# Kernel optimization log

Measured on AMD Instinct MI355X. Metric: run time of the kernel, lower is better.

## Reference

```python
import jax, jax.numpy as jnp
import numpy as np

B, T, H, V, L = 128, 64, 256, 128, 2


def _gru_layer(x_seq, w_ih, w_hh, b_ih, b_hh):
    """PyTorch-convention GRU layer. x_seq: (B,T,Hin) -> (B,T,H), h_last (B,H)."""
    # Precompute input projections once for all timesteps: (B,T,3H)
    xp = jnp.einsum('bti,gi->btg', x_seq, w_ih) + b_ih

    def step(h, xp_t):
        hp = h @ w_hh.T + b_hh                      # (B,3H)
        xr, xz, xn = jnp.split(xp_t, 3, axis=-1)
        hr, hz, hn = jnp.split(hp, 3, axis=-1)
        r = jax.nn.sigmoid(xr + hr)
        z = jax.nn.sigmoid(xz + hz)
        n = jnp.tanh(xn + r * hn)
        h_new = (1.0 - z) * n + z * h
        return h_new, h_new

    h0 = jnp.zeros((x_seq.shape[0], w_hh.shape[1]), x_seq.dtype)
    h_last, ys = jax.lax.scan(step, h0, jnp.swapaxes(xp, 0, 1))  # scan over T
    return jnp.swapaxes(ys, 0, 1), h_last


def setup_inputs() -> dict:
    key = jax.random.key(0)
    ks = jax.random.split(key, 16)
    s = 1.0 / np.sqrt(H)

    def u(k, shape):
        return jax.random.uniform(k, shape, jnp.float32, -s, s)

    x = jax.random.randint(ks[0], (B, T), 0, V)
    embed = jax.random.normal(ks[1], (V, H), jnp.float32) * 0.02
    embed = embed.at[0].set(0.0)  # padding_idx=0
    return {
        'x': x,
        'embed': embed,
        'w_ih0': u(ks[2], (3 * H, H)), 'w_hh0': u(ks[3], (3 * H, H)),
        'b_ih0': u(ks[4], (3 * H,)),   'b_hh0': u(ks[5], (3 * H,)),
        'w_ih1': u(ks[6], (3 * H, H)), 'w_hh1': u(ks[7], (3 * H, H)),
        'b_ih1': u(ks[8], (3 * H,)),   'b_hh1': u(ks[9], (3 * H,)),
        'W_a': u(ks[10], (H, H)),
        'U_a': u(ks[11], (H, H)),
        'v_a': u(ks[12], (H,)),
        'fc_W': u(ks[13], (V, 2 * H)),
        'fc_b': u(ks[14], (V,)),
    }


def reference(x, embed, w_ih0, w_hh0, b_ih0, b_hh0,
              w_ih1, w_hh1, b_ih1, b_hh1,
              W_a, U_a, v_a, fc_W, fc_b):
    # Embedding (dropout is identity in eval-mode reference)
    emb = embed[x]                                   # (B,T,H)
    h1_seq, _ = _gru_layer(emb, w_ih0, w_hh0, b_ih0, b_hh0)
    enc, h_last = _gru_layer(h1_seq, w_ih1, w_hh1, b_ih1, b_hh1)  # (B,T,H)

    # Vectorized per-step Bahdanau attention: queries are enc itself (h_t = enc[:,t])
    Wa_e = enc @ W_a.T                               # (B,T,H) keys, computed once
    Ua_h = enc @ U_a.T                               # (B,T,H) queries
    energy = jnp.einsum('btkh,h->btk',
                        jnp.tanh(Wa_e[:, None, :, :] + Ua_h[:, :, None, :]), v_a)
    alpha = jax.nn.softmax(energy, axis=-1)          # (B,T,T)
    ctx = jnp.einsum('btk,bkh->bth', alpha, enc)     # (B,T,H)

    combined = jnp.concatenate([enc, ctx], axis=-1)  # (B,T,2H)
    logits = combined @ fc_W.T + fc_b                # (B,T,V)
    return logits, h_last
```

## Files before the change

### kernel.cpp

```cpp
#include <hip/hip_runtime.h>
#include <math.h>

#define BB 128
#define TT 64
#define HH 256
#define G3 768
#define VV 128

typedef _Float16 half8 __attribute__((ext_vector_type(8)));
typedef float f32x4 __attribute__((ext_vector_type(4)));

__global__ __launch_bounds__(256) void pack_whh_f16(const float* __restrict__ w,
                                                    _Float16* __restrict__ out) {
    int d = blockIdx.x * 256 + threadIdx.x;
    int e   = d & 7;
    int l   = (d >> 3) & 63;
    int kap = (d >> 9) & 7;
    int wt  = d >> 12;
    int wv  = wt / 6, tau = wt % 6;
    int ncol = (tau >> 1) * 256 + wv * 32 + (tau & 1) * 16 + (l & 15);
    int k    = kap * 32 + (l >> 4) * 8 + e;
    out[d] = (_Float16)w[ncol * HH + k];
}

__global__ __launch_bounds__(256) void prep_bias(const float* __restrict__ b_ih,
                                                 const float* __restrict__ b_hh,
                                                 float* __restrict__ outb) {
    int j = blockIdx.x * 256 + threadIdx.x;
    outb[j] = b_ih[j] + (j < 2 * HH ? b_hh[j] : 0.f);
}

__global__ __launch_bounds__(256) void gemm_bt(
    const float* __restrict__ A1, int lda1, int K1,
    const float* __restrict__ A2, int lda2, int K2,
    const float* __restrict__ Bw, int ldb,
    const float* __restrict__ bias,
    float* __restrict__ C, int ldc, int M, int N)
{
    __shared__ alignas(16) float As[16][68];
    __shared__ alignas(16) float Bs[16][68];
    const int tid = threadIdx.x;
    const int lc = tid & 15, lr = tid >> 4;
    const int ty = tid >> 4, tx = tid & 15;
    const int row0 = blockIdx.y * 64, col0 = blockIdx.x * 64;
    float acc[4][4] = {};
    const int KT = K1 + K2;

    for (int k0 = 0; k0 < KT; k0 += 16) {
        const float* Ap; int lda, kk0;
        if (k0 < K1) { Ap = A1; lda = lda1; kk0 = k0; }
        else         { Ap = A2; lda = lda2; kk0 = k0 - K1; }
#pragma unroll
        for (int r = 0; r < 4; ++r) {
            As[lc][lr + 16 * r] = Ap[(row0 + lr + 16 * r) * lda + kk0 + lc];
            Bs[lc][lr + 16 * r] = Bw[(col0 + lr + 16 * r) * ldb + k0 + lc];
        }
        __syncthreads();
#pragma unroll
        for (int kk = 0; kk < 16; ++kk) {
            const float4 a4 = *(const float4*)&As[kk][ty * 4];
            const float4 b4 = *(const float4*)&Bs[kk][tx * 4];
            const float av[4] = {a4.x, a4.y, a4.z, a4.w};
            const float bv[4] = {b4.x, b4.y, b4.z, b4.w};
#pragma unroll
            for (int i = 0; i < 4; ++i)
#pragma unroll
                for (int j = 0; j < 4; ++j)
                    acc[i][j] += av[i] * bv[j];
        }
        __syncthreads();
    }

    float bv[4];
#pragma unroll
    for (int j = 0; j < 4; ++j)
        bv[j] = bias ? bias[col0 + tx * 4 + j] : 0.f;
#pragma unroll
    for (int i = 0; i < 4; ++i) {
        const int r = row0 + ty * 4 + i;
        float4 o;
        o.x = acc[i][0] + bv[0];
        o.y = acc[i][1] + bv[1];
        o.z = acc[i][2] + bv[2];
        o.w = acc[i][3] + bv[3];
        *(float4*)&C[r * ldc + col0 + tx * 4] = o;
    }
}

__global__ __launch_bounds__(512, 2) void gru_mfma(
    const _Float16* __restrict__ wp,
    const float* __restrict__ b_hh,
    const float* __restrict__ xsrc,
    const int*   __restrict__ xidx,
    float* __restrict__ out_seq,
    float* __restrict__ hlast,
    int mode)
{
    __shared__ alignas(16) _Float16 hbuf[16][264];
    __shared__ int tok[16][TT];
    const int tid = threadIdx.x;
    const int wv = tid >> 6, l = tid & 63;
    const int l15 = l & 15, lhi = l >> 4;
    const int r0 = blockIdx.x * 16;

    for (int i = tid; i < 16 * 264; i += 512) ((_Float16*)hbuf)[i] = (_Float16)0.f;
    if (mode == 0) {
        ((int*)tok)[tid]       = xidx[r0 * TT + tid];
        ((int*)tok)[tid + 512] = xidx[r0 * TT + tid + 512];
    }

    half8 W[48];
    const half8* wp8 = (const half8*)wp;
    const int fb = wv * 48 * 64;
#pragma unroll
    for (int f = 0; f < 48; ++f) W[f] = wp8[fb + f * 64 + l];

    const int colbase = wv * 32 + l15;
    const float bhn0 = b_hh[2 * HH + colbase];
    const float bhn1 = b_hh[2 * HH + colbase + 16];
    float hold[2][4] = {};
    __syncthreads();

    for (int t = 0; t < TT; ++t) {
        f32x4 acc[6];
#pragma unroll
        for (int tau = 0; tau < 6; ++tau) acc[tau] = (f32x4)0.f;

#pragma unroll
        for (int kap = 0; kap < 8; ++kap) {
            const half8 a = *(const half8*)&hbuf[l15][kap * 32 + lhi * 8];
#pragma unroll
            for (int tau = 0; tau < 6; ++tau)
                acc[tau] = __builtin_amdgcn_mfma_f32_16x16x32_f16(
                    a, W[tau * 8 + kap], acc[tau], 0, 0, 0);
        }
        __syncthreads();

#pragma unroll
        for (int s = 0; s < 2; ++s) {
            const int col = colbase + s * 16;
            const float bhn = s ? bhn1 : bhn0;
            float xr[4], xz[4], xn[4];
#pragma unroll
            for (int reg = 0; reg < 4; ++reg) {
                const int rr = lhi * 4 + reg;
                const long base = (mode == 0)
                    ? (long)tok[rr][t] * G3
                    : (long)((r0 + rr) * TT + t) * G3;
                xr[reg] = xsrc[base + col];
                xz[reg] = xsrc[base + col + HH];
                xn[reg] = xsrc[base + col + 2 * HH];
            }
#pragma unroll
            for (int reg = 0; reg < 4; ++reg) {
                const int row = lhi * 4 + reg;
                const float pr = acc[0 + s][reg] + xr[reg];
                const float pz = acc[2 + s][reg] + xz[reg];
                const float hn = acc[4 + s][reg] + bhn;
                const float rg = 1.f / (1.f + __expf(-pr));
                const float zg = 1.f / (1.f + __expf(-pz));
                const float npre = xn[reg] + rg * hn;
                const float e2 = __expf(2.f * npre);
                const float ng = (e2 - 1.f) / (e2 + 1.f);
                const float hnew = (1.f - zg) * ng + zg * hold[s][reg];
                hold[s][reg] = hnew;
                hbuf[row][col] = (_Float16)hnew;
                const int brow = r0 + row;
                out_seq[(brow * TT + t) * HH + col] = hnew;
                if (mode == 1 && t == TT - 1) hlast[brow * HH + col] = hnew;
            }
        }
        __syncthreads();
    }
}

__device__ __forceinline__ float tanh_fast(float x) {
    const float e = __expf(2.f * x);
    return (e - 1.f) / (e + 1.f);
}

__global__ __launch_bounds__(256) void attn_kernel(
    const float* __restrict__ WU,
    const float* __restrict__ enc,
    const float* __restrict__ v_a,
    float* __restrict__ ctx)
{
    __shared__ float q[HH], va[HH], sm[TT];
    const int tid = threadIdx.x;
    const int t = blockIdx.x, b = blockIdx.y;

    q[tid]  = WU[(b * TT + t) * 512 + 256 + tid];
    va[tid] = v_a[tid];
    __syncthreads();

    const int w = tid >> 6, lane = tid & 63;
#pragma unroll 4
    for (int i = 0; i < 16; ++i) {
        const int k = w * 16 + i;
        const float* we = WU + (b * TT + k) * 512;
        float s = 0.f;
#pragma unroll
        for (int c = 0; c < 4; ++c) {
            const int h = lane + 64 * c;
            s += va[h] * tanh_fast(we[h] + q[h]);
        }
#pragma unroll
        for (int off = 32; off > 0; off >>= 1) s += __shfl_xor(s, off);
        if (lane == 0) sm[k] = s;
    }
    __syncthreads();

    if (tid < TT) {
        const float e = sm[tid];
        float mx = e;
#pragma unroll
        for (int off = 32; off > 0; off >>= 1) mx = fmaxf(mx, __shfl_xor(mx, off));
        const float p = __expf(e - mx);
        float sum = p;
#pragma unroll
        for (int off = 32; off > 0; off >>= 1) sum += __shfl_xor(sum, off);
        sm[tid] = p / sum;
    }
    __syncthreads();

    float c = 0.f;
    for (int k = 0; k < TT; ++k)
        c += sm[k] * enc[(b * TT + k) * HH + tid];
    ctx[(b * TT + t) * HH + tid] = c;
}

extern "C" void kernel_launch(void* const* d_in, const int* in_sizes, int n_in,
                              void* d_out, int out_size, void* d_ws, size_t ws_size,
                              hipStream_t stream) {
    const int*   x     = (const int*)  d_in[0];
    const float* embed = (const float*)d_in[1];
    const float* w_ih0 = (const float*)d_in[2];
    const float* w_hh0 = (const float*)d_in[3];
    const float* b_ih0 = (const float*)d_in[4];
    const float* b_hh0 = (const float*)d_in[5];
    const float* w_ih1 = (const float*)d_in[6];
    const float* w_hh1 = (const float*)d_in[7];
    const float* b_ih1 = (const float*)d_in[8];
    const float* b_hh1 = (const float*)d_in[9];
    const float* W_a   = (const float*)d_in[10];
    const float* U_a   = (const float*)d_in[11];
    const float* v_a   = (const float*)d_in[12];
    const float* fc_W  = (const float*)d_in[13];
    const float* fc_b  = (const float*)d_in[14];
    float* out = (float*)d_out;

    float* ws = (float*)d_ws;
    _Float16* wT0 = (_Float16*)ws;
    _Float16* wT1 = wT0 + 196608;
    float* bias0 = ws    + 196608;
    float* bias1 = bias0 + 768;
    float* P0    = bias1 + 768;
    float* h1    = P0    + 98304;
    float* xp1   = h1    + 2097152;
    float* enc   = xp1   + 6291456;
    float* WU_B  = enc   + 2097152;
    float* WU    = WU_B  + 131072;
    float* ctxb  = WU    + 4194304;

    float* logits = out;
    float* hlast  = out + BB * TT * VV;

    pack_whh_f16<<<768, 256, 0, stream>>>(w_hh0, wT0);
    pack_whh_f16<<<768, 256, 0, stream>>>(w_hh1, wT1);
    prep_bias<<<3, 256, 0, stream>>>(b_ih0, b_hh0, bias0);
    prep_bias<<<3, 256, 0, stream>>>(b_ih1, b_hh1, bias1);
    hipMemcpyAsync(WU_B, W_a, HH * HH * sizeof(float),
                   hipMemcpyDeviceToDevice, stream);
    hipMemcpyAsync(WU_B + HH * HH, U_a, HH * HH * sizeof(float),
                   hipMemcpyDeviceToDevice, stream);

    gemm_bt<<<dim3(G3 / 64, VV / 64), 256, 0, stream>>>(
        embed, HH, HH, nullptr, 0, 0, w_ih0, HH, bias0, P0, G3, VV, G3);

    gru_mfma<<<BB / 16, 512, 0, stream>>>(wT0, b_hh0, P0, x, h1, nullptr, 0);

    gemm_bt<<<dim3(G3 / 64, BB * TT / 64), 256, 0, stream>>>(
        h1, HH, HH, nullptr, 0, 0, w_ih1, HH, bias1, xp1, G3, BB * TT, G3);

    gru_mfma<<<BB / 16, 512, 0, stream>>>(wT1, b_hh1, xp1, nullptr, enc, hlast, 1);

    gemm_bt<<<dim3(512 / 64, BB * TT / 64), 256, 0, stream>>>(
        enc, HH, HH, nullptr, 0, 0, WU_B, HH, nullptr, WU, 512, BB * TT, 512);

    attn_kernel<<<dim3(TT, BB), 256, 0, stream>>>(WU, enc, v_a, ctxb);

    gemm_bt<<<dim3(VV / 64, BB * TT / 64), 256, 0, stream>>>(
        enc, HH, HH, ctxb, HH, HH, fc_W, 2 * HH, fc_b, logits, VV, BB * TT, VV);
}
```

Measured before the change: 679.9 us.

## Prefetch GRU input projections one step ahead and double-buffer hidden state

The input-projection GEMM now writes its output interleaved as [row][col][gate] padded to 4 floats, and for layer 1 in a time-major order. Each GRU lane can then fetch r, z and n for a column with a single float4 load. The recurrent kernel loads the next timestep's projections into registers while the current step's MFMAs run. It also double-buffers the fp16 hidden state in LDS, which removes one __syncthreads per step. The cost is more registers in a kernel already holding 48 weight fragments, strided scalar stores in the GEMM epilogue, and a workspace layout where xp1 and WU share the same memory.

```diff
diff --git a/kernel.cpp b/kernel.cpp
--- a/kernel.cpp
+++ b/kernel.cpp
@@ -35,7 +35,7 @@
     const float* __restrict__ A2, int lda2, int K2,
     const float* __restrict__ Bw, int ldb,
     const float* __restrict__ bias,
-    float* __restrict__ C, int ldc, int M, int N)
+    float* __restrict__ C, int ldc, int M, int N, int permmode)
 {
     __shared__ alignas(16) float As[16][68];
     __shared__ alignas(16) float Bs[16][68];
@@ -78,12 +78,22 @@
 #pragma unroll
     for (int i = 0; i < 4; ++i) {
         const int r = row0 + ty * 4 + i;
-        float4 o;
-        o.x = acc[i][0] + bv[0];
-        o.y = acc[i][1] + bv[1];
-        o.z = acc[i][2] + bv[2];
-        o.w = acc[i][3] + bv[3];
-        *(float4*)&C[r * ldc + col0 + tx * 4] = o;
+        if (permmode == 0) {
+            float4 o;
+            o.x = acc[i][0] + bv[0];
+            o.y = acc[i][1] + bv[1];
+            o.z = acc[i][2] + bv[2];
+            o.w = acc[i][3] + bv[3];
+            *(float4*)&C[r * ldc + col0 + tx * 4] = o;
+        } else {
+            const int orow = (permmode == 2) ? ((r & 63) * BB + (r >> 6)) : r;
+#pragma unroll
+            for (int jj = 0; jj < 4; ++jj) {
+                const int j = col0 + tx * 4 + jj;
+                const int g = j >> 8, c = j & 255;
+                C[orow * 1024 + c * 4 + g] = acc[i][jj] + bv[jj];
+            }
+        }
     }
 }
 
@@ -96,14 +106,14 @@
     float* __restrict__ hlast,
     int mode)
 {
-    __shared__ alignas(16) _Float16 hbuf[16][264];
+    __shared__ alignas(16) _Float16 hbuf[2][16][264];
     __shared__ int tok[16][TT];
     const int tid = threadIdx.x;
     const int wv = tid >> 6, l = tid & 63;
     const int l15 = l & 15, lhi = l >> 4;
     const int r0 = blockIdx.x * 16;
 
-    for (int i = tid; i < 16 * 264; i += 512) ((_Float16*)hbuf)[i] = (_Float16)0.f;
+    for (int i = tid; i < 16 * 264; i += 512) ((_Float16*)hbuf[0])[i] = (_Float16)0.f;
     if (mode == 0) {
         ((int*)tok)[tid]       = xidx[r0 * TT + tid];
         ((int*)tok)[tid + 512] = xidx[r0 * TT + tid + 512];
@@ -121,55 +131,79 @@
     float hold[2][4] = {};
     __syncthreads();
 
+    float4 xqA[2][4], xqB[2][4];
+#pragma unroll
+    for (int s = 0; s < 2; ++s) {
+        const int c = colbase + 16 * s;
+#pragma unroll
+        for (int reg = 0; reg < 4; ++reg) {
+            const int rr = lhi * 4 + reg;
+            const long row = (mode == 0) ? (long)tok[rr][0] : (long)(r0 + rr);
+            xqA[s][reg] = *(const float4*)&xsrc[row * 1024 + c * 4];
+        }
+    }
+
+    int cur = 0;
     for (int t = 0; t < TT; ++t) {
+        if (t + 1 < TT) {
+#pragma unroll
+            for (int s = 0; s < 2; ++s) {
+                const int c = colbase + 16 * s;
+#pragma unroll
+                for (int reg = 0; reg < 4; ++reg) {
+                    const int rr = lhi * 4 + reg;
+                    const long row = (mode == 0)
+                        ? (long)tok[rr][t + 1]
+                        : (long)(t + 1) * BB + (r0 + rr);
+                    xqB[s][reg] = *(const float4*)&xsrc[row * 1024 + c * 4];
+                }
+            }
+        }
+
         f32x4 acc[6];
 #pragma unroll
         for (int tau = 0; tau < 6; ++tau) acc[tau] = (f32x4)0.f;
 
 #pragma unroll
         for (int kap = 0; kap < 8; ++kap) {
-            const half8 a = *(const half8*)&hbuf[l15][kap * 32 + lhi * 8];
+            const half8 a = *(const half8*)&hbuf[cur][l15][kap * 32 + lhi * 8];
 #pragma unroll
             for (int tau = 0; tau < 6; ++tau)
                 acc[tau] = __builtin_amdgcn_mfma_f32_16x16x32_f16(
                     a, W[tau * 8 + kap], acc[tau], 0, 0, 0);
         }
-        __syncthreads();
 
 #pragma unroll
         for (int s = 0; s < 2; ++s) {
             const int col = colbase + s * 16;
             const float bhn = s ? bhn1 : bhn0;
-            float xr[4], xz[4], xn[4];
-#pragma unroll
-            for (int reg = 0; reg < 4; ++reg) {
-                const int rr = lhi * 4 + reg;
-                const long base = (mode == 0)
-                    ? (long)tok[rr][t] * G3
-                    : (long)((r0 + rr) * TT + t) * G3;
-                xr[reg] = xsrc[base + col];
-                xz[reg] = xsrc[base + col + HH];
-                xn[reg] = xsrc[base + col + 2 * HH];
-            }
 #pragma unroll
             for (int reg = 0; reg < 4; ++reg) {
                 const int row = lhi * 4 + reg;
-                const float pr = acc[0 + s][reg] + xr[reg];
-                const float pz = acc[2 + s][reg] + xz[reg];
+                const float pr = acc[0 + s][reg] + xqA[s][reg].x;
+                const float pz = acc[2 + s][reg] + xqA[s][reg].y;
                 const float hn = acc[4 + s][reg] + bhn;
                 const float rg = 1.f / (1.f + __expf(-pr));
                 const float zg = 1.f / (1.f + __expf(-pz));
-                const float npre = xn[reg] + rg * hn;
+                const float npre = xqA[s][reg].z + rg * hn;
                 const float e2 = __expf(2.f * npre);
                 const float ng = (e2 - 1.f) / (e2 + 1.f);
                 const float hnew = (1.f - zg) * ng + zg * hold[s][reg];
                 hold[s][reg] = hnew;
-                hbuf[row][col] = (_Float16)hnew;
+                hbuf[cur ^ 1][row][col] = (_Float16)hnew;
                 const int brow = r0 + row;
                 out_seq[(brow * TT + t) * HH + col] = hnew;
                 if (mode == 1 && t == TT - 1) hlast[brow * HH + col] = hnew;
             }
         }
+
+#pragma unroll
+        for (int s = 0; s < 2; ++s)
+#pragma unroll
+            for (int reg = 0; reg < 4; ++reg)
+                xqA[s][reg] = xqB[s][reg];
+
+        cur ^= 1;
         __syncthreads();
     }
 }
@@ -255,12 +289,12 @@
     float* bias0 = ws    + 196608;
     float* bias1 = bias0 + 768;
     float* P0    = bias1 + 768;
-    float* h1    = P0    + 98304;
-    float* xp1   = h1    + 2097152;
-    float* enc   = xp1   + 6291456;
+    float* h1    = P0    + 131072;
+    float* enc   = h1    + 2097152;
     float* WU_B  = enc   + 2097152;
-    float* WU    = WU_B  + 131072;
-    float* ctxb  = WU    + 4194304;
+    float* xp1   = WU_B  + 131072;
+    float* WU    = xp1;
+    float* ctxb  = xp1   + 4194304;
 
     float* logits = out;
     float* hlast  = out + BB * TT * VV;
@@ -275,20 +309,20 @@
                    hipMemcpyDeviceToDevice, stream);
 
     gemm_bt<<<dim3(G3 / 64, VV / 64), 256, 0, stream>>>(
-        embed, HH, HH, nullptr, 0, 0, w_ih0, HH, bias0, P0, G3, VV, G3);
+        embed, HH, HH, nullptr, 0, 0, w_ih0, HH, bias0, P0, 0, VV, G3, 1);
 
     gru_mfma<<<BB / 16, 512, 0, stream>>>(wT0, b_hh0, P0, x, h1, nullptr, 0);
 
     gemm_bt<<<dim3(G3 / 64, BB * TT / 64), 256, 0, stream>>>(
-        h1, HH, HH, nullptr, 0, 0, w_ih1, HH, bias1, xp1, G3, BB * TT, G3);
+        h1, HH, HH, nullptr, 0, 0, w_ih1, HH, bias1, xp1, 0, BB * TT, G3, 2);
 
     gru_mfma<<<BB / 16, 512, 0, stream>>>(wT1, b_hh1, xp1, nullptr, enc, hlast, 1);
 
     gemm_bt<<<dim3(512 / 64, BB * TT / 64), 256, 0, stream>>>(
-        enc, HH, HH, nullptr, 0, 0, WU_B, HH, nullptr, WU, 512, BB * TT, 512);
+        enc, HH, HH, nullptr, 0, 0, WU_B, HH, nullptr, WU, 512, BB * TT, 512, 0);
 
     attn_kernel<<<dim3(TT, BB), 256, 0, stream>>>(WU, enc, v_a, ctxb);
 
     gemm_bt<<<dim3(VV / 64, BB * TT / 64), 256, 0, stream>>>(
-        enc, HH, HH, ctxb, HH, HH, fc_W, 2 * HH, fc_b, logits, VV, BB * TT, VV);
-}
+        enc, HH, HH, ctxb, HH, HH, fc_W, 2 * HH, fc_b, logits, VV, BB * TT, VV, 0);
+}
```

New measurement: 985.1 us. +44.9%, slower.

## Convert projection GEMMs to fp16 MFMA and store intermediates in half precision

Applied to the files above, without the earlier changes.

Replaces the scalar fp32 tiled GEMM with an fp16 MFMA-based GEMM, casting weights and embeddings to fp16 up front. Intermediate activations (xp, h1, enc, ctx) are stored in fp16 to halve memory traffic. The layer-1 input projection is written time-major so the recurrent kernel reads each step's rows contiguously. This reduces GEMM compute and bandwidth cost, but adds several cast kernels and fp16 rounding error in the activations.

```diff
diff --git a/kernel.cpp b/kernel.cpp
--- a/kernel.cpp
+++ b/kernel.cpp
@@ -8,7 +8,18 @@
 #define VV 128
 
 typedef _Float16 half8 __attribute__((ext_vector_type(8)));
+typedef _Float16 half4v __attribute__((ext_vector_type(4)));
 typedef float f32x4 __attribute__((ext_vector_type(4)));
+
+__global__ __launch_bounds__(256) void cast_f16(const float* __restrict__ in,
+                                                _Float16* __restrict__ out, int n4) {
+    int i = blockIdx.x * 256 + threadIdx.x;
+    if (i < n4) {
+        float4 v = ((const float4*)in)[i];
+        half4v h = {(_Float16)v.x, (_Float16)v.y, (_Float16)v.z, (_Float16)v.w};
+        ((half4v*)out)[i] = h;
+    }
+}
 
 __global__ __launch_bounds__(256) void pack_whh_f16(const float* __restrict__ w,
                                                     _Float16* __restrict__ out) {
@@ -30,69 +41,66 @@
     outb[j] = b_ih[j] + (j < 2 * HH ? b_hh[j] : 0.f);
 }
 
-__global__ __launch_bounds__(256) void gemm_bt(
-    const float* __restrict__ A1, int lda1, int K1,
-    const float* __restrict__ A2, int lda2, int K2,
-    const float* __restrict__ Bw, int ldb,
+__global__ __launch_bounds__(256) void gemm_f16(
+    const _Float16* __restrict__ A1, int lda1, int K1,
+    const _Float16* __restrict__ A2, int lda2, int K2,
+    const _Float16* __restrict__ Bw, int ldb,
     const float* __restrict__ bias,
-    float* __restrict__ C, int ldc, int M, int N)
+    void* __restrict__ Cv, int ldc, int M, int N, int omode)
 {
-    __shared__ alignas(16) float As[16][68];
-    __shared__ alignas(16) float Bs[16][68];
+    __shared__ alignas(16) _Float16 As[64][36];
+    __shared__ alignas(16) _Float16 Bs[64][36];
     const int tid = threadIdx.x;
-    const int lc = tid & 15, lr = tid >> 4;
-    const int ty = tid >> 4, tx = tid & 15;
+    const int wv = tid >> 6, l = tid & 63;
+    const int l15 = l & 15, lhi = l >> 4;
     const int row0 = blockIdx.y * 64, col0 = blockIdx.x * 64;
-    float acc[4][4] = {};
+    const int ar = tid >> 2, ac = (tid & 3) * 8;
     const int KT = K1 + K2;
 
-    for (int k0 = 0; k0 < KT; k0 += 16) {
-        const float* Ap; int lda, kk0;
+    f32x4 acc[4];
+#pragma unroll
+    for (int m = 0; m < 4; ++m) acc[m] = (f32x4)0.f;
+
+    for (int k0 = 0; k0 < KT; k0 += 32) {
+        const _Float16* Ap; int lda, kk0;
         if (k0 < K1) { Ap = A1; lda = lda1; kk0 = k0; }
         else         { Ap = A2; lda = lda2; kk0 = k0 - K1; }
-#pragma unroll
-        for (int r = 0; r < 4; ++r) {
-            As[lc][lr + 16 * r] = Ap[(row0 + lr + 16 * r) * lda + kk0 + lc];
-            Bs[lc][lr + 16 * r] = Bw[(col0 + lr + 16 * r) * ldb + k0 + lc];
-        }
+        *(half8*)&As[ar][ac] = *(const half8*)&Ap[(long)(row0 + ar) * lda + kk0 + ac];
+        *(half8*)&Bs[ar][ac] = *(const half8*)&Bw[(long)(col0 + ar) * ldb + k0 + ac];
         __syncthreads();
-#pragma unroll
-        for (int kk = 0; kk < 16; ++kk) {
-            const float4 a4 = *(const float4*)&As[kk][ty * 4];
-            const float4 b4 = *(const float4*)&Bs[kk][tx * 4];
-            const float av[4] = {a4.x, a4.y, a4.z, a4.w};
-            const float bv[4] = {b4.x, b4.y, b4.z, b4.w};
-#pragma unroll
-            for (int i = 0; i < 4; ++i)
-#pragma unroll
-                for (int j = 0; j < 4; ++j)
-                    acc[i][j] += av[i] * bv[j];
+        const half8 bfrag = *(const half8*)&Bs[wv * 16 + l15][lhi * 8];
+#pragma unroll
+        for (int m = 0; m < 4; ++m) {
+            const half8 afrag = *(const half8*)&As[m * 16 + l15][lhi * 8];
+            acc[m] = __builtin_amdgcn_mfma_f32_16x16x32_f16(afrag, bfrag, acc[m], 0, 0, 0);
         }
         __syncthreads();
     }
 
-    float bv[4];
-#pragma unroll
-    for (int j = 0; j < 4; ++j)
-        bv[j] = bias ? bias[col0 + tx * 4 + j] : 0.f;
-#pragma unroll
-    for (int i = 0; i < 4; ++i) {
-        const int r = row0 + ty * 4 + i;
-        float4 o;
-        o.x = acc[i][0] + bv[0];
-        o.y = acc[i][1] + bv[1];
-        o.z = acc[i][2] + bv[2];
-        o.w = acc[i][3] + bv[3];
-        *(float4*)&C[r * ldc + col0 + tx * 4] = o;
+    const int col = col0 + wv * 16 + l15;
+    const float bb = bias ? bias[col] : 0.f;
+#pragma unroll
+    for (int m = 0; m < 4; ++m) {
+#pragma unroll
+        for (int reg = 0; reg < 4; ++reg) {
+            const int r = row0 + m * 16 + lhi * 4 + reg;
+            const float v = acc[m][reg] + bb;
+            if (omode == 0) {
+                ((float*)Cv)[(long)r * ldc + col] = v;
+            } else {
+                const int orow = (omode == 2) ? ((r & 63) * BB + (r >> 6)) : r;
+                ((_Float16*)Cv)[(long)orow * ldc + col] = (_Float16)v;
+            }
+        }
     }
 }
 
 __global__ __launch_bounds__(512, 2) void gru_mfma(
     const _Float16* __restrict__ wp,
     const float* __restrict__ b_hh,
-    const float* __restrict__ xsrc,
+    const _Float16* __restrict__ xsrc,
     const int*   __restrict__ xidx,
-    float* __restrict__ out_seq,
+    _Float16* __restrict__ out_seq,
     float* __restrict__ hlast,
     int mode)
 {
@@ -140,34 +148,28 @@
         for (int s = 0; s < 2; ++s) {
             const int col = colbase + s * 16;
             const float bhn = s ? bhn1 : bhn0;
-            float xr[4], xz[4], xn[4];
-#pragma unroll
-            for (int reg = 0; reg < 4; ++reg) {
-                const int rr = lhi * 4 + reg;
-                const long base = (mode == 0)
-                    ? (long)tok[rr][t] * G3
-                    : (long)((r0 + rr) * TT + t) * G3;
-                xr[reg] = xsrc[base + col];
-                xz[reg] = xsrc[base + col + HH];
-                xn[reg] = xsrc[base + col + 2 * HH];
-            }
 #pragma unroll
             for (int reg = 0; reg < 4; ++reg) {
                 const int row = lhi * 4 + reg;
-                const float pr = acc[0 + s][reg] + xr[reg];
-                const float pz = acc[2 + s][reg] + xz[reg];
+                const long base = (mode == 0)
+                    ? (long)tok[row][t] * G3
+                    : ((long)t * BB + (r0 + row)) * G3;
+                const float xr  = (float)xsrc[base + col];
+                const float xz  = (float)xsrc[base + col + HH];
+                const float xnv = (float)xsrc[base + col + 2 * HH];
+                const float pr = acc[0 + s][reg] + xr;
+                const float pz = acc[2 + s][reg] + xz;
                 const float hn = acc[4 + s][reg] + bhn;
                 const float rg = 1.f / (1.f + __expf(-pr));
                 const float zg = 1.f / (1.f + __expf(-pz));
-                const float npre = xn[reg] + rg * hn;
+                const float npre = xnv + rg * hn;
                 const float e2 = __expf(2.f * npre);
                 const float ng = (e2 - 1.f) / (e2 + 1.f);
                 const float hnew = (1.f - zg) * ng + zg * hold[s][reg];
                 hold[s][reg] = hnew;
                 hbuf[row][col] = (_Float16)hnew;
-                const int brow = r0 + row;
-                out_seq[(brow * TT + t) * HH + col] = hnew;
-                if (mode == 1 && t == TT - 1) hlast[brow * HH + col] = hnew;
+                out_seq[((long)(r0 + row) * TT + t) * HH + col] = (_Float16)hnew;
+                if (mode == 1 && t == TT - 1) hlast[(r0 + row) * HH + col] = hnew;
             }
         }
         __syncthreads();
@@ -181,9 +183,9 @@
 
 __global__ __launch_bounds__(256) void attn_kernel(
     const float* __restrict__ WU,
-    const float* __restrict__ enc,
+    const _Float16* __restrict__ enc,
     const float* __restrict__ v_a,
-    float* __restrict__ ctx)
+    _Float16* __restrict__ ctx)
 {
     __shared__ float q[HH], va[HH], sm[TT];
     const int tid = threadIdx.x;
@@ -225,8 +227,8 @@
 
     float c = 0.f;
     for (int k = 0; k < TT; ++k)
-        c += sm[k] * enc[(b * TT + k) * HH + tid];
-    ctx[(b * TT + t) * HH + tid] = c;
+        c += sm[k] * (float)enc[(b * TT + k) * HH + tid];
+    ctx[(b * TT + t) * HH + tid] = (_Float16)c;
 }
 
 extern "C" void kernel_launch(void* const* d_in, const int* in_sizes, int n_in,
@@ -250,45 +252,51 @@
     float* out = (float*)d_out;
 
     float* ws = (float*)d_ws;
-    _Float16* wT0 = (_Float16*)ws;
-    _Float16* wT1 = wT0 + 196608;
-    float* bias0 = ws    + 196608;
-    float* bias1 = bias0 + 768;
-    float* P0    = bias1 + 768;
-    float* h1    = P0    + 98304;
-    float* xp1   = h1    + 2097152;
-    float* enc   = xp1   + 6291456;
-    float* WU_B  = enc   + 2097152;
-    float* WU    = WU_B  + 131072;
-    float* ctxb  = WU    + 4194304;
+    _Float16* wT0    = (_Float16*)ws;
+    _Float16* wT1    = (_Float16*)(ws + 98304);
+    float*    bias0  = ws + 196608;
+    float*    bias1  = ws + 197376;
+    _Float16* embh   = (_Float16*)(ws + 198144);
+    _Float16* wih0h  = (_Float16*)(ws + 214528);
+    _Float16* wih1h  = (_Float16*)(ws + 312832);
+    _Float16* WUBh   = (_Float16*)(ws + 411136);
+    _Float16* fcWh   = (_Float16*)(ws + 476672);
+    _Float16* P0h    = (_Float16*)(ws + 509440);
+    _Float16* h1h    = (_Float16*)(ws + 558592);
+    _Float16* ench   = (_Float16*)(ws + 1607168);
+    _Float16* ctxh   = (_Float16*)(ws + 2655744);
+    _Float16* xp1h   = (_Float16*)(ws + 3704320);
+    float*    WU     = ws + 3704320;
 
     float* logits = out;
     float* hlast  = out + BB * TT * VV;
 
+    cast_f16<<<32, 256, 0, stream>>>(embed, embh, VV * HH / 4);
+    cast_f16<<<192, 256, 0, stream>>>(w_ih0, wih0h, G3 * HH / 4);
+    cast_f16<<<192, 256, 0, stream>>>(w_ih1, wih1h, G3 * HH / 4);
+    cast_f16<<<64, 256, 0, stream>>>(W_a, WUBh, HH * HH / 4);
+    cast_f16<<<64, 256, 0, stream>>>(U_a, WUBh + HH * HH, HH * HH / 4);
+    cast_f16<<<64, 256, 0, stream>>>(fc_W, fcWh, VV * 2 * HH / 4);
     pack_whh_f16<<<768, 256, 0, stream>>>(w_hh0, wT0);
     pack_whh_f16<<<768, 256, 0, stream>>>(w_hh1, wT1);
     prep_bias<<<3, 256, 0, stream>>>(b_ih0, b_hh0, bias0);
     prep_bias<<<3, 256, 0, stream>>>(b_ih1, b_hh1, bias1);
-    hipMemcpyAsync(WU_B, W_a, HH * HH * sizeof(float),
-                   hipMemcpyDeviceToDevice, stream);
-    hipMemcpyAsync(WU_B + HH * HH, U_a, HH * HH * sizeof(float),
-                   hipMemcpyDeviceToDevice, stream);
-
-    gemm_bt<<<dim3(G3 / 64, VV / 64), 256, 0, stream>>>(
-        embed, HH, HH, nullptr, 0, 0, w_ih0, HH, bias0, P0, G3, VV, G3);
-
-    gru_mfma<<<BB / 16, 512, 0, stream>>>(wT0, b_hh0, P0, x, h1, nullptr, 0);
-
-    gemm_bt<<<dim3(G3 / 64, BB * TT / 64), 256, 0, stream>>>(
-        h1, HH, HH, nullptr, 0, 0, w_ih1, HH, bias1, xp1, G3, BB * TT, G3);
-
-    gru_mfma<<<BB / 16, 512, 0, stream>>>(wT1, b_hh1, xp1, nullptr, enc, hlast, 1);
-
-    gemm_bt<<<dim3(512 / 64, BB * TT / 64), 256, 0, stream>>>(
-        enc, HH, HH, nullptr, 0, 0, WU_B, HH, nullptr, WU, 512, BB * TT, 512);
-
-    attn_kernel<<<dim3(TT, BB), 256, 0, stream>>>(WU, enc, v_a, ctxb);
-
-    gemm_bt<<<dim3(VV / 64, BB * TT / 64), 256, 0, stream>>>(
-        enc, HH, HH, ctxb, HH, HH, fc_W, 2 * HH, fc_b, logits, VV, BB * TT, VV);
-}
+
+    gemm_f16<<<dim3(G3 / 64, VV / 64), 256, 0, stream>>>(
+        embh, HH, HH, nullptr, 0, 0, wih0h, HH, bias0, P0h, G3, VV, G3, 1);
+
+    gru_mfma<<<BB / 16, 512, 0, stream>>>(wT0, b_hh0, P0h, x, h1h, nullptr, 0);
+
+    gemm_f16<<<dim3(G3 / 64, BB * TT / 64), 256, 0, stream>>>(
+        h1h, HH, HH, nullptr, 0, 0, wih1h, HH, bias1, xp1h, G3, BB * TT, G3, 2);
+
+    gru_mfma<<<BB / 16, 512, 0, stream>>>(wT1, b_hh1, xp1h, nullptr, ench, hlast, 1);
+
+    gemm_f16<<<dim3(512 / 64, BB * TT / 64), 256, 0, stream>>>(
+        ench, HH, HH, nullptr, 0, 0, WUBh, HH, nullptr, WU, 512, BB * TT, 512, 0);
+
+    attn_kernel<<<dim3(TT, BB), 256, 0, stream>>>(WU, ench, v_a, ctxh);
+
+    gemm_f16<<<dim3(VV / 64, BB * TT / 64), 256, 0, stream>>>(
+        ench, HH, HH, ctxh, HH, HH, fcWh, 2 * HH, fc_b, logits, VV, BB * TT, VV, 0);
+}
```

New measurement: 730.3 us. 1.07x slower.
